# Kernel tuning notes

Hardware: AMD Instinct MI355X
Metric: run time of the kernel (lower is better)

The kernel has to match this reference:

```python
import jax, jax.numpy as jnp
import numpy as np

T, B, D, HID, L = 256, 64, 1024, 1024, 2


def setup_inputs() -> dict:
    key = jax.random.key(0)
    k1, k2, k3 = jax.random.split(key, 3)
    X = jax.random.normal(k1, (T, B, D), dtype=jnp.float32)
    # Stacked gate weights in order (i, f, o, c); xavier-like scale.
    Wx = jax.random.normal(k2, (L, 4 * HID, D), dtype=jnp.float32) * 0.03
    Wh = jax.random.normal(k3, (L, 4 * HID, HID), dtype=jnp.float32) * 0.03
    # Combined bias (Linear bias + b_gate); forget-gate bias initialized to 1.
    b = jnp.zeros((L, 4 * HID), dtype=jnp.float32).at[:, HID:2 * HID].set(1.0)
    return {"X": X, "Wx": Wx, "Wh": Wh, "b": b}


def reference(X, Wx, Wh, b):
    num_layers, H4, _ = Wx.shape
    Hd = H4 // 4
    Bsz = X.shape[1]
    H0 = jnp.zeros((num_layers, Bsz, Hd), X.dtype)
    C0 = jnp.zeros((num_layers, Bsz, Hd), X.dtype)

    def step(carry, x_t):
        H, C = carry
        x = x_t
        Hn, Cn = [], []
        for l in range(num_layers):  # small fixed layer count
            # fused gate GEMM: [B, 4H]
            g = x @ Wx[l].T + H[l] @ Wh[l].T + b[l]
            i_g, f_g, o_g, c_g = jnp.split(g, 4, axis=-1)
            c = jax.nn.sigmoid(f_g) * C[l] + jax.nn.sigmoid(i_g) * jnp.tanh(c_g)
            h = jax.nn.sigmoid(o_g) * jnp.tanh(c)
            Hn.append(h)
            Cn.append(c)
            x = h  # dropout is identity in eval mode
        return (jnp.stack(Hn), jnp.stack(Cn)), x

    (Hf, Cf), outputs = jax.lax.scan(step, (H0, C0), X)
    return outputs, Hf, Cf
```

## Files before the change

### kernel.cpp

```cpp
#include <hip/hip_runtime.h>
#include <cstdint>
#include <cstddef>

typedef __attribute__((ext_vector_type(8))) short short8;
typedef __attribute__((ext_vector_type(4))) float floatx4;
typedef unsigned short u16;
typedef unsigned long long u64;

#define NSTEP 256

__device__ __forceinline__ unsigned f2b_rne(float x) {
  unsigned u = __builtin_bit_cast(unsigned, x);
  return (u + 0x7fffu + ((u >> 16) & 1u)) >> 16;
}
__device__ __forceinline__ float b2f(u16 b) {
  unsigned u = ((unsigned)b) << 16;
  return __builtin_bit_cast(float, u);
}
__device__ __forceinline__ float sigf(float x) {
  x = fminf(fmaxf(x, -30.f), 30.f);
  return __builtin_amdgcn_rcpf(1.f + __expf(-x));
}
__device__ __forceinline__ float tanhf_fast(float x) {
  x = fminf(fmaxf(x, -15.f), 15.f);
  float e = __expf(2.f * x);
  return (e - 1.f) * __builtin_amdgcn_rcpf(e + 1.f);
}

__device__ __forceinline__ unsigned ald(const unsigned* p) {
  return __hip_atomic_load(p, __ATOMIC_RELAXED, __HIP_MEMORY_SCOPE_AGENT);
}
__device__ __forceinline__ void ast(unsigned* p, unsigned v) {
  __hip_atomic_store(p, v, __ATOMIC_RELAXED, __HIP_MEMORY_SCOPE_AGENT);
}

__global__ void init_kernel(unsigned* h0, unsigned* h1) {
  int i = blockIdx.x * blockDim.x + threadIdx.x;
  if (i < 32768) { h0[i] = 0; h1[i] = 0; }
}

__global__ void init2_kernel(unsigned* fl) {
  int i = blockIdx.x * blockDim.x + threadIdx.x;
  if (i < 2048) fl[i] = 0;
}

__global__ void cast_kernel(const float* __restrict__ in, u16* __restrict__ out, int n4) {
  int i = blockIdx.x * blockDim.x + threadIdx.x;
  int stride = gridDim.x * blockDim.x;
  for (; i < n4; i += stride) {
    float4 v = ((const float4*)in)[i];
    unsigned lo = f2b_rne(v.x) | (f2b_rne(v.y) << 16);
    unsigned hi = f2b_rne(v.z) | (f2b_rne(v.w) << 16);
    ((uint2*)out)[i] = make_uint2(lo, hi);
  }
}

#define GEMM_Q(HROW, W)                                                        \
  {                                                                            \
    short8 a_[8][4];                                                           \
    _Pragma("unroll")                                                          \
    for (int c_ = 0; c_ < 8; ++c_) {                                           \
      int k_ = kq0 + c_ * 32 + q * 8;                                          \
      const unsigned* base_ = (HROW) + (k_ >> 4) * 512 + ((k_ & 15) >> 1);     \
      _Pragma("unroll")                                                        \
      for (int m_ = 0; m_ < 4; ++m_)                                           \
        a_[c_][m_] = *(const short8*)(base_ + (m_ * 16 + n16) * 8);            \
    }                                                                          \
    _Pragma("unroll")                                                          \
    for (int c_ = 0; c_ < 8; ++c_)                                             \
      _Pragma("unroll")                                                        \
      for (int m_ = 0; m_ < 4; ++m_)                                           \
        asm volatile("" : "+v"(a_[c_][m_]));                                   \
    _Pragma("unroll")                                                          \
    for (int c_ = 0; c_ < 8; ++c_)                                             \
      _Pragma("unroll")                                                        \
      for (int m_ = 0; m_ < 4; ++m_)                                           \
        _Pragma("unroll")                                                      \
        for (int g_ = 0; g_ < 4; ++g_)                                         \
          acc[m_][g_] = __builtin_amdgcn_mfma_f32_16x16x32_bf16(a_[c_][m_], (W)[g_][c_], acc[m_][g_], 0, 0, 0); \
  }

#define GEMM_QX(XROW, W)                                                       \
  {                                                                            \
    short8 a_[8][4];                                                           \
    _Pragma("unroll")                                                          \
    for (int c_ = 0; c_ < 8; ++c_) {                                           \
      int k_ = kq0 + c_ * 32 + q * 8;                                          \
      _Pragma("unroll")                                                        \
      for (int m_ = 0; m_ < 4; ++m_)                                           \
        a_[c_][m_] = *(const short8*)((XROW) + (size_t)(m_ * 16 + n16) * 1024 + k_); \
    }                                                                          \
    _Pragma("unroll")                                                          \
    for (int c_ = 0; c_ < 8; ++c_)                                             \
      _Pragma("unroll")                                                        \
      for (int m_ = 0; m_ < 4; ++m_)                                           \
        asm volatile("" : "+v"(a_[c_][m_]));                                   \
    _Pragma("unroll")                                                          \
    for (int c_ = 0; c_ < 8; ++c_)                                             \
      _Pragma("unroll")                                                        \
      for (int m_ = 0; m_ < 4; ++m_)                                           \
        _Pragma("unroll")                                                      \
        for (int g_ = 0; g_ < 4; ++g_)                                         \
          acc[m_][g_] = __builtin_amdgcn_mfma_f32_16x16x32_bf16(a_[c_][m_], (W)[g_][c_], acc[m_][g_], 0, 0, 0); \
  }

#define REDUCE_TOT()                                                           \
  _Pragma("unroll")                                                            \
  for (int m_ = 0; m_ < 4; ++m_) {                                             \
    if (m_ != wv) {                                                            \
      int slot_ = (m_ - (m_ > wv ? 1 : 0)) * 4;                                \
      _Pragma("unroll")                                                        \
      for (int g_ = 0; g_ < 4; ++g_)                                           \
        *(floatx4*)&red[wv][slot_ + g_][lane * 4] = acc[m_][g_];               \
    }                                                                          \
  }                                                                            \
  __syncthreads();                                                             \
  _Pragma("unroll")                                                            \
  for (int g_ = 0; g_ < 4; ++g_) tot[g_] = acc[wv][g_];                        \
  _Pragma("unroll")                                                            \
  for (int w2_ = 0; w2_ < 4; ++w2_) {                                          \
    if (w2_ != wv) {                                                           \
      int slot_ = (wv - (wv > w2_ ? 1 : 0)) * 4;                               \
      _Pragma("unroll")                                                        \
      for (int g_ = 0; g_ < 4; ++g_)                                           \
        tot[g_] += *(const floatx4*)&red[w2_][slot_ + g_][lane * 4];           \
    }                                                                          \
  }

#define POLL1(FLA, TGTA)                                                       \
  if (wv == 0) {                                                               \
    int spins_ = 0;                                                            \
    for (;;) {                                                                 \
      unsigned va_ = ald((FLA) + lane * 8);                                    \
      if (__all((int)(va_ >= (TGTA)))) break;                                  \
      __builtin_amdgcn_s_sleep(1);                                             \
      if (++spins_ > (1 << 17)) break;                                         \
    }                                                                          \
  }
#define POLL2(FLA, TGTA, FLB, TGTB)                                            \
  if (wv == 0) {                                                               \
    int spins_ = 0;                                                            \
    for (;;) {                                                                 \
      unsigned va_ = ald((FLA) + lane * 8);                                    \
      unsigned vb_ = ald((FLB) + lane * 8);                                    \
      if (__all((int)((va_ >= (TGTA)) & (vb_ >= (TGTB))))) break;              \
      __builtin_amdgcn_s_sleep(1);                                             \
      if (++spins_ > (1 << 17)) break;                                         \
    }                                                                          \
  }

__global__ __launch_bounds__(256, 1) void lstm_fused(
    const u16* __restrict__ Wh0b,
    const u16* __restrict__ Wx0b,
    const u16* __restrict__ Wx1b,
    const u16* __restrict__ Wh1b,
    const u16* __restrict__ Xb,
    const float* __restrict__ bias,
    unsigned* H0u,
    unsigned* H1u,
    unsigned* G0u,
    unsigned* G1u,
    unsigned* FL,
    float* __restrict__ outp,
    float* __restrict__ hf,
    float* __restrict__ cf) {
  __shared__ float red[4][12][256];
  const int tid = threadIdx.x;
  const int wv = tid >> 6;
  const int lane = tid & 63;
  const int q = lane >> 4;
  const int n16 = lane & 15;
  const int gid = blockIdx.x >> 6;
  const int jb = blockIdx.x & 63;
  const int jg = (jb << 4) + n16;
  const int kq0 = wv << 8;
  unsigned* fl0 = FL;
  unsigned* fl1 = FL + 512;
  unsigned* fl2 = FL + 1024;
  unsigned* fl3 = FL + 1536;
  const floatx4 vzero = {0.f, 0.f, 0.f, 0.f};

  if (gid == 0) {
    short8 wf[4][8];
#pragma unroll
    for (int g = 0; g < 4; ++g)
#pragma unroll
      for (int c = 0; c < 8; ++c)
        wf[g][c] = *(const short8*)(Wh0b + (size_t)(g * 1024 + jg) * 1024 + kq0 + c * 32 + q * 8);
#pragma unroll
    for (int g = 0; g < 4; ++g)
#pragma unroll
      for (int c = 0; c < 8; ++c) asm volatile("" : "+v"(wf[g][c]));

    float bs[4];
#pragma unroll
    for (int g = 0; g < 4; ++g) bs[g] = bias[g * 1024 + jg];
    float cst[4] = {0.f, 0.f, 0.f, 0.f};

    for (int t = 0; t < NSTEP; ++t) {
      POLL2(fl0, (unsigned)t, fl3, (unsigned)(t + 1));
      __syncthreads();

      const unsigned* g0i = G0u + (size_t)(t & 7) * 131072 + jb * 2048;
      float gf[4][4];
#pragma unroll
      for (int g = 0; g < 4; ++g)
#pragma unroll
        for (int r = 0; r < 4; ++r) {
          int b = wv * 16 + q * 4 + r;
          unsigned dw = ald(g0i + g * 512 + b * 8 + (n16 >> 1));
          gf[g][r] = b2f((u16)(dw >> (16 * (n16 & 1))));
        }

      floatx4 acc[4][4];
#pragma unroll
      for (int m = 0; m < 4; ++m)
#pragma unroll
        for (int g = 0; g < 4; ++g) acc[m][g] = vzero;
      GEMM_Q(H0u + (size_t)t * 32768, wf);

      floatx4 tot[4];
      REDUCE_TOT();

      unsigned* hnext = H0u + (size_t)(t + 1) * 32768 + jb * 512;
      float hsv[4];
#pragma unroll
      for (int r = 0; r < 4; ++r) {
        float pi = tot[0][r] + gf[0][r] + bs[0];
        float pf = tot[1][r] + gf[1][r] + bs[1];
        float po = tot[2][r] + gf[2][r] + bs[2];
        float pc = tot[3][r] + gf[3][r] + bs[3];
        float cn = sigf(pf) * cst[r] + sigf(pi) * tanhf_fast(pc);
        float h = sigf(po) * tanhf_fast(cn);
        cst[r] = cn;
        hsv[r] = h;
        int brow = wv * 16 + q * 4 + r;
        unsigned hv = f2b_rne(h);
        unsigned pv = (unsigned)__shfl_xor((int)hv, 1);
        if (!(n16 & 1)) ast(hnext + brow * 8 + (n16 >> 1), hv | (pv << 16));
      }

      __syncthreads();
      if (tid == 0) ast(fl0 + jb * 8, (unsigned)(t + 1));

      if (t == NSTEP - 1) {
#pragma unroll
        for (int r = 0; r < 4; ++r) {
          int brow = wv * 16 + q * 4 + r;
          hf[brow * 1024 + jg] = hsv[r];
          cf[brow * 1024 + jg] = cst[r];
        }
      }
    }
  } else if (gid == 1) {
    short8 wf[4][8];
#pragma unroll
    for (int g = 0; g < 4; ++g)
#pragma unroll
      for (int c = 0; c < 8; ++c)
        wf[g][c] = *(const short8*)(Wx0b + (size_t)(g * 1024 + jg) * 1024 + kq0 + c * 32 + q * 8);
#pragma unroll
    for (int g = 0; g < 4; ++g)
#pragma unroll
      for (int c = 0; c < 8; ++c) asm volatile("" : "+v"(wf[g][c]));

    for (int t = 0; t < NSTEP; ++t) {
      unsigned tgtb = (t >= 8) ? (unsigned)(t - 7) : 0u;
      POLL1(fl0, tgtb);
      __syncthreads();

      floatx4 acc[4][4];
#pragma unroll
      for (int m = 0; m < 4; ++m)
#pragma unroll
        for (int g = 0; g < 4; ++g) acc[m][g] = vzero;
      GEMM_QX(Xb + (size_t)t * 65536, wf);

      floatx4 tot[4];
      REDUCE_TOT();

      unsigned* g0o = G0u + (size_t)(t & 7) * 131072 + jb * 2048;
#pragma unroll
      for (int r = 0; r < 4; ++r) {
        int b = wv * 16 + q * 4 + r;
#pragma unroll
        for (int g = 0; g < 4; ++g) {
          unsigned v = f2b_rne(tot[g][r]);
          unsigned pv = (unsigned)__shfl_xor((int)v, 1);
          if (!(n16 & 1)) ast(g0o + g * 512 + b * 8 + (n16 >> 1), v | (pv << 16));
        }
      }

      __syncthreads();
      if (tid == 0) ast(fl3 + jb * 8, (unsigned)(t + 1));
    }
  } else if (gid == 2) {
    short8 wf[4][8];
#pragma unroll
    for (int g = 0; g < 4; ++g)
#pragma unroll
      for (int c = 0; c < 8; ++c)
        wf[g][c] = *(const short8*)(Wx1b + (size_t)(g * 1024 + jg) * 1024 + kq0 + c * 32 + q * 8);
#pragma unroll
    for (int g = 0; g < 4; ++g)
#pragma unroll
      for (int c = 0; c < 8; ++c) asm volatile("" : "+v"(wf[g][c]));

    for (int t = 0; t < NSTEP; ++t) {
      unsigned tgtb = (t >= 8) ? (unsigned)(t - 7) : 0u;
      POLL2(fl0, (unsigned)(t + 1), fl1, tgtb);
      __syncthreads();

      floatx4 acc[4][4];
#pragma unroll
      for (int m = 0; m < 4; ++m)
#pragma unroll
        for (int g = 0; g < 4; ++g) acc[m][g] = vzero;
      GEMM_Q(H0u + (size_t)(t + 1) * 32768, wf);

      floatx4 tot[4];
      REDUCE_TOT();

      unsigned* g1o = G1u + (size_t)(t & 7) * 131072 + jb * 2048;
#pragma unroll
      for (int r = 0; r < 4; ++r) {
        int b = wv * 16 + q * 4 + r;
#pragma unroll
        for (int g = 0; g < 4; ++g) {
          unsigned v = f2b_rne(tot[g][r]);
          unsigned pv = (unsigned)__shfl_xor((int)v, 1);
          if (!(n16 & 1)) ast(g1o + g * 512 + b * 8 + (n16 >> 1), v | (pv << 16));
        }
      }

      __syncthreads();
      if (tid == 0) ast(fl2 + jb * 8, (unsigned)(t + 1));
    }
  } else {
    short8 wf[4][8];
#pragma unroll
    for (int g = 0; g < 4; ++g)
#pragma unroll
      for (int c = 0; c < 8; ++c)
        wf[g][c] = *(const short8*)(Wh1b + (size_t)(g * 1024 + jg) * 1024 + kq0 + c * 32 + q * 8);
#pragma unroll
    for (int g = 0; g < 4; ++g)
#pragma unroll
      for (int c = 0; c < 8; ++c) asm volatile("" : "+v"(wf[g][c]));

    float bs[4];
#pragma unroll
    for (int g = 0; g < 4; ++g) bs[g] = bias[4096 + g * 1024 + jg];
    float cst[4] = {0.f, 0.f, 0.f, 0.f};

    for (int t = 0; t < NSTEP; ++t) {
      POLL2(fl2, (unsigned)(t + 1), fl1, (unsigned)t);
      __syncthreads();

      const unsigned* g1i = G1u + (size_t)(t & 7) * 131072 + jb * 2048;
      float gf[4][4];
#pragma unroll
      for (int g = 0; g < 4; ++g)
#pragma unroll
        for (int r = 0; r < 4; ++r) {
          int b = wv * 16 + q * 4 + r;
          unsigned dw = ald(g1i + g * 512 + b * 8 + (n16 >> 1));
          gf[g][r] = b2f((u16)(dw >> (16 * (n16 & 1))));
        }

      floatx4 acc[4][4];
#pragma unroll
      for (int m = 0; m < 4; ++m)
#pragma unroll
        for (int g = 0; g < 4; ++g) acc[m][g] = vzero;
      GEMM_Q(H1u + (size_t)t * 32768, wf);

      floatx4 tot[4];
      REDUCE_TOT();

      unsigned* hnext = H1u + (size_t)(t + 1) * 32768 + jb * 512;
      float hsv[4];
#pragma unroll
      for (int r = 0; r < 4; ++r) {
        float pi = tot[0][r] + gf[0][r] + bs[0];
        float pf = tot[1][r] + gf[1][r] + bs[1];
        float po = tot[2][r] + gf[2][r] + bs[2];
        float pc = tot[3][r] + gf[3][r] + bs[3];
        float cn = sigf(pf) * cst[r] + sigf(pi) * tanhf_fast(pc);
        float h = sigf(po) * tanhf_fast(cn);
        cst[r] = cn;
        hsv[r] = h;
        int brow = wv * 16 + q * 4 + r;
        unsigned hv = f2b_rne(h);
        unsigned pv = (unsigned)__shfl_xor((int)hv, 1);
        if (!(n16 & 1)) ast(hnext + brow * 8 + (n16 >> 1), hv | (pv << 16));
      }

      __syncthreads();
      if (tid == 0) ast(fl1 + jb * 8, (unsigned)(t + 1));

#pragma unroll
      for (int r = 0; r < 4; ++r) {
        int brow = wv * 16 + q * 4 + r;
        outp[((size_t)t * 64 + brow) * 1024 + jg] = hsv[r];
      }
      if (t == NSTEP - 1) {
#pragma unroll
        for (int r = 0; r < 4; ++r) {
          int brow = wv * 16 + q * 4 + r;
          hf[65536 + brow * 1024 + jg] = hsv[r];
          cf[65536 + brow * 1024 + jg] = cst[r];
        }
      }
    }
  }
}

extern "C" void kernel_launch(void* const* d_in, const int* in_sizes, int n_in,
                              void* d_out, int out_size, void* d_ws, size_t ws_size,
                              hipStream_t stream) {
  const float* X  = (const float*)d_in[0];
  const float* Wx = (const float*)d_in[1];
  const float* Wh = (const float*)d_in[2];
  const float* b  = (const float*)d_in[3];
  float* out = (float*)d_out;

  char* ws = (char*)d_ws;
  u16* Xbf  = (u16*)(ws);
  u16* Wxbf = (u16*)(ws + 33554432);
  u16* Whbf = (u16*)(ws + 50331648);
  unsigned* H0 = (unsigned*)(ws + 67108864);
  unsigned* H1 = (unsigned*)(ws + 100794368);
  unsigned* G0 = (unsigned*)(ws + 134479872);
  unsigned* G1 = (unsigned*)(ws + 138674176);
  unsigned* FL = (unsigned*)(ws + 142868480);

  float* out_seq = out;
  float* Hf = out + 16777216;
  float* Cf = out + 16777216 + 131072;

  init_kernel<<<128, 256, 0, stream>>>(H0, H1);
  init2_kernel<<<8, 256, 0, stream>>>(FL);
  cast_kernel<<<2048, 256, 0, stream>>>(X, Xbf, 16777216 / 4);
  cast_kernel<<<2048, 256, 0, stream>>>(Wx, Wxbf, 8388608 / 4);
  cast_kernel<<<2048, 256, 0, stream>>>(Wh, Whbf, 8388608 / 4);

  lstm_fused<<<256, 256, 0, stream>>>(Whbf, Wxbf, Wxbf + 4194304, Whbf + 4194304,
                                      Xbf, b, H0, H1, G0, G1, FL, out_seq, Hf, Cf);
}
```

Before: 2.356 ms.

## Merge input-projection and recurrent blocks into one 512-thread block per layer slice

The four separate 256-thread block groups (layer-0 recurrent, layer-0 input projection, layer-1 input projection, layer-1 recurrent) become 128 blocks of 512 threads. One half of each block computes the recurrent GEMM, and the other half precomputes the next step's input-projection gates into a double-buffered LDS array (gbuf). This removes the global bf16 G0/G1 gate buffers, their flags and cross-block polling, and keeps the gate pre-activations in fp32 in shared memory. The cost is a block-wide barrier that couples both halves every step, plus tighter lookahead: the input projection now runs only one step ahead instead of up to eight.

```diff
diff --git a/kernel.cpp b/kernel.cpp
--- a/kernel.cpp
+++ b/kernel.cpp
@@ -107,23 +107,23 @@
 #define REDUCE_TOT()                                                           \
   _Pragma("unroll")                                                            \
   for (int m_ = 0; m_ < 4; ++m_) {                                             \
-    if (m_ != wv) {                                                            \
-      int slot_ = (m_ - (m_ > wv ? 1 : 0)) * 4;                                \
+    if (m_ != wq) {                                                            \
+      int slot_ = (m_ - (m_ > wq ? 1 : 0)) * 4;                                \
       _Pragma("unroll")                                                        \
       for (int g_ = 0; g_ < 4; ++g_)                                           \
-        *(floatx4*)&red[wv][slot_ + g_][lane * 4] = acc[m_][g_];               \
+        *(floatx4*)&redh[wq][slot_ + g_][lane * 4] = acc[m_][g_];              \
     }                                                                          \
   }                                                                            \
   __syncthreads();                                                             \
   _Pragma("unroll")                                                            \
-  for (int g_ = 0; g_ < 4; ++g_) tot[g_] = acc[wv][g_];                        \
+  for (int g_ = 0; g_ < 4; ++g_) tot[g_] = acc[wq][g_];                        \
   _Pragma("unroll")                                                            \
   for (int w2_ = 0; w2_ < 4; ++w2_) {                                          \
-    if (w2_ != wv) {                                                           \
-      int slot_ = (wv - (wv > w2_ ? 1 : 0)) * 4;                               \
+    if (w2_ != wq) {                                                           \
+      int slot_ = (wq - (wq > w2_ ? 1 : 0)) * 4;                               \
       _Pragma("unroll")                                                        \
       for (int g_ = 0; g_ < 4; ++g_)                                           \
-        tot[g_] += *(const floatx4*)&red[w2_][slot_ + g_][lane * 4];           \
+        tot[g_] += *(const floatx4*)&redh[w2_][slot_ + g_][lane * 4];          \
     }                                                                          \
   }
 
@@ -149,7 +149,7 @@
     }                                                                          \
   }
 
-__global__ __launch_bounds__(256, 1) void lstm_fused(
+__global__ __launch_bounds__(512, 2) void lstm_fused(
     const u16* __restrict__ Wh0b,
     const u16* __restrict__ Wx0b,
     const u16* __restrict__ Wx1b,
@@ -158,258 +158,143 @@
     const float* __restrict__ bias,
     unsigned* H0u,
     unsigned* H1u,
-    unsigned* G0u,
-    unsigned* G1u,
     unsigned* FL,
     float* __restrict__ outp,
     float* __restrict__ hf,
     float* __restrict__ cf) {
-  __shared__ float red[4][12][256];
+  __shared__ float redL[4][12][256];
+  __shared__ float redP[4][12][256];
+  __shared__ float gbuf[2][4][64][18];
   const int tid = threadIdx.x;
   const int wv = tid >> 6;
+  const int half = wv >> 2;
+  const int wq = wv & 3;
   const int lane = tid & 63;
   const int q = lane >> 4;
   const int n16 = lane & 15;
-  const int gid = blockIdx.x >> 6;
+  const int grp = blockIdx.x >> 6;
   const int jb = blockIdx.x & 63;
   const int jg = (jb << 4) + n16;
-  const int kq0 = wv << 8;
+  const int kq0 = wq << 8;
   unsigned* fl0 = FL;
   unsigned* fl1 = FL + 512;
-  unsigned* fl2 = FL + 1024;
-  unsigned* fl3 = FL + 1536;
+  unsigned* flme = grp ? fl1 : fl0;
+  unsigned* Hme = grp ? H1u : H0u;
+  float (*redh)[12][256] = half ? redP : redL;
   const floatx4 vzero = {0.f, 0.f, 0.f, 0.f};
 
-  if (gid == 0) {
-    short8 wf[4][8];
-#pragma unroll
-    for (int g = 0; g < 4; ++g)
-#pragma unroll
-      for (int c = 0; c < 8; ++c)
-        wf[g][c] = *(const short8*)(Wh0b + (size_t)(g * 1024 + jg) * 1024 + kq0 + c * 32 + q * 8);
-#pragma unroll
-    for (int g = 0; g < 4; ++g)
-#pragma unroll
-      for (int c = 0; c < 8; ++c) asm volatile("" : "+v"(wf[g][c]));
-
-    float bs[4];
-#pragma unroll
-    for (int g = 0; g < 4; ++g) bs[g] = bias[g * 1024 + jg];
-    float cst[4] = {0.f, 0.f, 0.f, 0.f};
-
-    for (int t = 0; t < NSTEP; ++t) {
-      POLL2(fl0, (unsigned)t, fl3, (unsigned)(t + 1));
-      __syncthreads();
-
-      const unsigned* g0i = G0u + (size_t)(t & 7) * 131072 + jb * 2048;
-      float gf[4][4];
-#pragma unroll
-      for (int g = 0; g < 4; ++g)
-#pragma unroll
-        for (int r = 0; r < 4; ++r) {
-          int b = wv * 16 + q * 4 + r;
-          unsigned dw = ald(g0i + g * 512 + b * 8 + (n16 >> 1));
-          gf[g][r] = b2f((u16)(dw >> (16 * (n16 & 1))));
-        }
-
-      floatx4 acc[4][4];
-#pragma unroll
-      for (int m = 0; m < 4; ++m)
-#pragma unroll
-        for (int g = 0; g < 4; ++g) acc[m][g] = vzero;
-      GEMM_Q(H0u + (size_t)t * 32768, wf);
-
-      floatx4 tot[4];
-      REDUCE_TOT();
-
-      unsigned* hnext = H0u + (size_t)(t + 1) * 32768 + jb * 512;
-      float hsv[4];
+  const u16* Wmy = half ? (grp ? Wx1b : Wx0b) : (grp ? Wh1b : Wh0b);
+  short8 wf[4][8];
+#pragma unroll
+  for (int g = 0; g < 4; ++g)
+#pragma unroll
+    for (int c = 0; c < 8; ++c)
+      wf[g][c] = *(const short8*)(Wmy + (size_t)(g * 1024 + jg) * 1024 + kq0 + c * 32 + q * 8);
+#pragma unroll
+  for (int g = 0; g < 4; ++g)
+#pragma unroll
+    for (int c = 0; c < 8; ++c) asm volatile("" : "+v"(wf[g][c]));
+
+  float bs[4] = {0.f, 0.f, 0.f, 0.f};
+  if (half == 0) {
+#pragma unroll
+    for (int g = 0; g < 4; ++g) bs[g] = bias[grp * 4096 + g * 1024 + jg];
+  }
+  float cst[4] = {0.f, 0.f, 0.f, 0.f};
+
+  if (grp == 1) { POLL1(fl0, 1u); }
+  __syncthreads();
+  {
+    floatx4 acc[4][4];
+#pragma unroll
+    for (int m = 0; m < 4; ++m)
+#pragma unroll
+      for (int g = 0; g < 4; ++g) acc[m][g] = vzero;
+    if (half == 1) {
+      if (grp == 0) { GEMM_QX(Xb, wf); }
+      else          { GEMM_Q(H0u + 32768, wf); }
+    }
+    floatx4 tot[4];
+    REDUCE_TOT();
+    if (half == 1) {
 #pragma unroll
       for (int r = 0; r < 4; ++r) {
-        float pi = tot[0][r] + gf[0][r] + bs[0];
-        float pf = tot[1][r] + gf[1][r] + bs[1];
-        float po = tot[2][r] + gf[2][r] + bs[2];
-        float pc = tot[3][r] + gf[3][r] + bs[3];
+        int b = wq * 16 + q * 4 + r;
+#pragma unroll
+        for (int g = 0; g < 4; ++g) gbuf[0][g][b][n16] = tot[g][r];
+      }
+    }
+  }
+
+  for (int t = 0; t < NSTEP; ++t) {
+    if (grp == 0) {
+      POLL1(fl0, (unsigned)t);
+    } else {
+      unsigned t0 = (unsigned)((t + 2 > NSTEP) ? NSTEP : t + 2);
+      POLL2(fl1, (unsigned)t, fl0, t0);
+    }
+    __syncthreads();
+
+    floatx4 acc[4][4];
+#pragma unroll
+    for (int m = 0; m < 4; ++m)
+#pragma unroll
+      for (int g = 0; g < 4; ++g) acc[m][g] = vzero;
+
+    if (half == 0) {
+      GEMM_Q(Hme + (size_t)t * 32768, wf);
+    } else if (t + 1 < NSTEP) {
+      if (grp == 0) { GEMM_QX(Xb + (size_t)(t + 1) * 65536, wf); }
+      else          { GEMM_Q(H0u + (size_t)(t + 2) * 32768, wf); }
+    }
+
+    floatx4 tot[4];
+    REDUCE_TOT();
+
+    float hsv[4];
+    if (half == 0) {
+      unsigned* hnext = Hme + (size_t)(t + 1) * 32768 + jb * 512;
+#pragma unroll
+      for (int r = 0; r < 4; ++r) {
+        int b = wq * 16 + q * 4 + r;
+        float pi = tot[0][r] + gbuf[t & 1][0][b][n16] + bs[0];
+        float pf = tot[1][r] + gbuf[t & 1][1][b][n16] + bs[1];
+        float po = tot[2][r] + gbuf[t & 1][2][b][n16] + bs[2];
+        float pc = tot[3][r] + gbuf[t & 1][3][b][n16] + bs[3];
         float cn = sigf(pf) * cst[r] + sigf(pi) * tanhf_fast(pc);
         float h = sigf(po) * tanhf_fast(cn);
         cst[r] = cn;
         hsv[r] = h;
-        int brow = wv * 16 + q * 4 + r;
         unsigned hv = f2b_rne(h);
         unsigned pv = (unsigned)__shfl_xor((int)hv, 1);
-        if (!(n16 & 1)) ast(hnext + brow * 8 + (n16 >> 1), hv | (pv << 16));
-      }
-
-      __syncthreads();
-      if (tid == 0) ast(fl0 + jb * 8, (unsigned)(t + 1));
-
+        if (!(n16 & 1)) ast(hnext + b * 8 + (n16 >> 1), hv | (pv << 16));
+      }
+    } else if (t + 1 < NSTEP) {
+#pragma unroll
+      for (int r = 0; r < 4; ++r) {
+        int b = wq * 16 + q * 4 + r;
+#pragma unroll
+        for (int g = 0; g < 4; ++g) gbuf[(t + 1) & 1][g][b][n16] = tot[g][r];
+      }
+    }
+
+    __syncthreads();
+    if (tid == 0) ast(flme + jb * 8, (unsigned)(t + 1));
+
+    if (half == 0) {
+      if (grp == 1) {
+#pragma unroll
+        for (int r = 0; r < 4; ++r) {
+          int b = wq * 16 + q * 4 + r;
+          outp[((size_t)t * 64 + b) * 1024 + jg] = hsv[r];
+        }
+      }
       if (t == NSTEP - 1) {
 #pragma unroll
         for (int r = 0; r < 4; ++r) {
-          int brow = wv * 16 + q * 4 + r;
-          hf[brow * 1024 + jg] = hsv[r];
-          cf[brow * 1024 + jg] = cst[r];
-        }
-      }
-    }
-  } else if (gid == 1) {
-    short8 wf[4][8];
-#pragma unroll
-    for (int g = 0; g < 4; ++g)
-#pragma unroll
-      for (int c = 0; c < 8; ++c)
-        wf[g][c] = *(const short8*)(Wx0b + (size_t)(g * 1024 + jg) * 1024 + kq0 + c * 32 + q * 8);
-#pragma unroll
-    for (int g = 0; g < 4; ++g)
-#pragma unroll
-      for (int c = 0; c < 8; ++c) asm volatile("" : "+v"(wf[g][c]));
-
-    for (int t = 0; t < NSTEP; ++t) {
-      unsigned tgtb = (t >= 8) ? (unsigned)(t - 7) : 0u;
-      POLL1(fl0, tgtb);
-      __syncthreads();
-
-      floatx4 acc[4][4];
-#pragma unroll
-      for (int m = 0; m < 4; ++m)
-#pragma unroll
-        for (int g = 0; g < 4; ++g) acc[m][g] = vzero;
-      GEMM_QX(Xb + (size_t)t * 65536, wf);
-
-      floatx4 tot[4];
-      REDUCE_TOT();
-
-      unsigned* g0o = G0u + (size_t)(t & 7) * 131072 + jb * 2048;
-#pragma unroll
-      for (int r = 0; r < 4; ++r) {
-        int b = wv * 16 + q * 4 + r;
-#pragma unroll
-        for (int g = 0; g < 4; ++g) {
-          unsigned v = f2b_rne(tot[g][r]);
-          unsigned pv = (unsigned)__shfl_xor((int)v, 1);
-          if (!(n16 & 1)) ast(g0o + g * 512 + b * 8 + (n16 >> 1), v | (pv << 16));
-        }
-      }
-
-      __syncthreads();
-      if (tid == 0) ast(fl3 + jb * 8, (unsigned)(t + 1));
-    }
-  } else if (gid == 2) {
-    short8 wf[4][8];
-#pragma unroll
-    for (int g = 0; g < 4; ++g)
-#pragma unroll
-      for (int c = 0; c < 8; ++c)
-        wf[g][c] = *(const short8*)(Wx1b + (size_t)(g * 1024 + jg) * 1024 + kq0 + c * 32 + q * 8);
-#pragma unroll
-    for (int g = 0; g < 4; ++g)
-#pragma unroll
-      for (int c = 0; c < 8; ++c) asm volatile("" : "+v"(wf[g][c]));
-
-    for (int t = 0; t < NSTEP; ++t) {
-      unsigned tgtb = (t >= 8) ? (unsigned)(t - 7) : 0u;
-      POLL2(fl0, (unsigned)(t + 1), fl1, tgtb);
-      __syncthreads();
-
-      floatx4 acc[4][4];
-#pragma unroll
-      for (int m = 0; m < 4; ++m)
-#pragma unroll
-        for (int g = 0; g < 4; ++g) acc[m][g] = vzero;
-      GEMM_Q(H0u + (size_t)(t + 1) * 32768, wf);
-
-      floatx4 tot[4];
-      REDUCE_TOT();
-
-      unsigned* g1o = G1u + (size_t)(t & 7) * 131072 + jb * 2048;
-#pragma unroll
-      for (int r = 0; r < 4; ++r) {
-        int b = wv * 16 + q * 4 + r;
-#pragma unroll
-        for (int g = 0; g < 4; ++g) {
-          unsigned v = f2b_rne(tot[g][r]);
-          unsigned pv = (unsigned)__shfl_xor((int)v, 1);
-          if (!(n16 & 1)) ast(g1o + g * 512 + b * 8 + (n16 >> 1), v | (pv << 16));
-        }
-      }
-
-      __syncthreads();
-      if (tid == 0) ast(fl2 + jb * 8, (unsigned)(t + 1));
-    }
-  } else {
-    short8 wf[4][8];
-#pragma unroll
-    for (int g = 0; g < 4; ++g)
-#pragma unroll
-      for (int c = 0; c < 8; ++c)
-        wf[g][c] = *(const short8*)(Wh1b + (size_t)(g * 1024 + jg) * 1024 + kq0 + c * 32 + q * 8);
-#pragma unroll
-    for (int g = 0; g < 4; ++g)
-#pragma unroll
-      for (int c = 0; c < 8; ++c) asm volatile("" : "+v"(wf[g][c]));
-
-    float bs[4];
-#pragma unroll
-    for (int g = 0; g < 4; ++g) bs[g] = bias[4096 + g * 1024 + jg];
-    float cst[4] = {0.f, 0.f, 0.f, 0.f};
-
-    for (int t = 0; t < NSTEP; ++t) {
-      POLL2(fl2, (unsigned)(t + 1), fl1, (unsigned)t);
-      __syncthreads();
-
-      const unsigned* g1i = G1u + (size_t)(t & 7) * 131072 + jb * 2048;
-      float gf[4][4];
-#pragma unroll
-      for (int g = 0; g < 4; ++g)
-#pragma unroll
-        for (int r = 0; r < 4; ++r) {
-          int b = wv * 16 + q * 4 + r;
-          unsigned dw = ald(g1i + g * 512 + b * 8 + (n16 >> 1));
-          gf[g][r] = b2f((u16)(dw >> (16 * (n16 & 1))));
-        }
-
-      floatx4 acc[4][4];
-#pragma unroll
-      for (int m = 0; m < 4; ++m)
-#pragma unroll
-        for (int g = 0; g < 4; ++g) acc[m][g] = vzero;
-      GEMM_Q(H1u + (size_t)t * 32768, wf);
-
-      floatx4 tot[4];
-      REDUCE_TOT();
-
-      unsigned* hnext = H1u + (size_t)(t + 1) * 32768 + jb * 512;
-      float hsv[4];
-#pragma unroll
-      for (int r = 0; r < 4; ++r) {
-        float pi = tot[0][r] + gf[0][r] + bs[0];
-        float pf = tot[1][r] + gf[1][r] + bs[1];
-        float po = tot[2][r] + gf[2][r] + bs[2];
-        float pc = tot[3][r] + gf[3][r] + bs[3];
-        float cn = sigf(pf) * cst[r] + sigf(pi) * tanhf_fast(pc);
-        float h = sigf(po) * tanhf_fast(cn);
-        cst[r] = cn;
-        hsv[r] = h;
-        int brow = wv * 16 + q * 4 + r;
-        unsigned hv = f2b_rne(h);
-        unsigned pv = (unsigned)__shfl_xor((int)hv, 1);
-        if (!(n16 & 1)) ast(hnext + brow * 8 + (n16 >> 1), hv | (pv << 16));
-      }
-
-      __syncthreads();
-      if (tid == 0) ast(fl1 + jb * 8, (unsigned)(t + 1));
-
-#pragma unroll
-      for (int r = 0; r < 4; ++r) {
-        int brow = wv * 16 + q * 4 + r;
-        outp[((size_t)t * 64 + brow) * 1024 + jg] = hsv[r];
-      }
-      if (t == NSTEP - 1) {
-#pragma unroll
-        for (int r = 0; r < 4; ++r) {
-          int brow = wv * 16 + q * 4 + r;
-          hf[65536 + brow * 1024 + jg] = hsv[r];
-          cf[65536 + brow * 1024 + jg] = cst[r];
+          int b = wq * 16 + q * 4 + r;
+          hf[grp * 65536 + b * 1024 + jg] = hsv[r];
+          cf[grp * 65536 + b * 1024 + jg] = cst[r];
         }
       }
     }
@@ -431,9 +316,7 @@
   u16* Whbf = (u16*)(ws + 50331648);
   unsigned* H0 = (unsigned*)(ws + 67108864);
   unsigned* H1 = (unsigned*)(ws + 100794368);
-  unsigned* G0 = (unsigned*)(ws + 134479872);
-  unsigned* G1 = (unsigned*)(ws + 138674176);
-  unsigned* FL = (unsigned*)(ws + 142868480);
+  unsigned* FL = (unsigned*)(ws + 134479872);
 
   float* out_seq = out;
   float* Hf = out + 16777216;
@@ -445,6 +328,6 @@
   cast_kernel<<<2048, 256, 0, stream>>>(Wx, Wxbf, 8388608 / 4);
   cast_kernel<<<2048, 256, 0, stream>>>(Wh, Whbf, 8388608 / 4);
 
-  lstm_fused<<<256, 256, 0, stream>>>(Whbf, Wxbf, Wxbf + 4194304, Whbf + 4194304,
-                                      Xbf, b, H0, H1, G0, G1, FL, out_seq, Hf, Cf);
-}
+  lstm_fused<<<128, 512, 0, stream>>>(Whbf, Wxbf, Wxbf + 4194304, Whbf + 4194304,
+                                      Xbf, b, H0, H1, FL, out_seq, Hf, Cf);
+}
```

Result: slower. 5.769 ms (+144.8%).
